# Performance work log

Measured on AMD Instinct MI355X. Metric: run time of the kernel, lower is better.

The kernel has to match this reference:

```python
import jax, jax.numpy as jnp
import numpy as np

GAMMA = 1.0        # soft-min temperature for differentiable DTW
BIG = 1e9          # value for cells outside the Sakoe-Chiba band
DTW_BW = 0.2       # band width as fraction of normalized path deviation
AVG_T_LEN = True   # divide discrepancy by input sequence length


def _softmin3(a, b, c):
    # differentiable min over the three DP predecessors
    z = jnp.stack([a, b, c], axis=0)
    return -GAMMA * jax.nn.logsumexp(-z / GAMMA, axis=0)


def _dtw(C, mask):
    """Band-limited soft-DTW DP. C: [T,K] pairwise costs, mask: [T,K] bool band.
    Returns scalar D[T-1,K-1]. Row scan over T; inner scan over K carries the
    left neighbor (recurrence D[i,j] = C[i,j] + softmin(D[i-1,j], D[i,j-1], D[i-1,j-1]))."""
    T, K = C.shape

    def row_step(carry, inp):
        prev_row, diag0 = carry            # prev_row: D[i-1,:]; diag0: virtual D[i-1,-1]
        c_row, m_row = inp
        diag = jnp.concatenate([diag0[None], prev_row[:-1]])  # D[i-1,j-1]

        def col_step(left, xs):
            c, up, dg, m = xs
            d = c + _softmin3(up, left, dg)
            d = jnp.where(m, d, BIG)       # kill cells outside the band
            return d, d

        _, row = jax.lax.scan(col_step, jnp.float32(BIG), (c_row, prev_row, diag, m_row))
        return (row, jnp.float32(BIG)), None

    # virtual border: D[-1,-1] = 0, all other border cells = BIG
    init = (jnp.full((K,), BIG, dtype=jnp.float32), jnp.float32(0.0))
    (last_row, _), _ = jax.lax.scan(row_step, init, (C, mask))
    return last_row[-1]


def setup_inputs() -> dict:
    key = jax.random.key(0)
    kx, kp = jax.random.split(key)
    B, T = 64, 512
    F, K = 32, 64
    x = jax.random.normal(kx, (B, T), dtype=jnp.float32)
    protos = jax.random.normal(kp, (F, K), dtype=jnp.float32)  # learnable DTW kernels
    return {"x": x, "protos": protos}


def reference(x, protos):
    B, T = x.shape
    F, K = protos.shape
    # pairwise squared costs: [B, F, T, K]
    C = (x[:, None, :, None] - protos[None, :, None, :]) ** 2
    # Sakoe-Chiba band on normalized coordinates
    ii = jnp.arange(T, dtype=jnp.float32) / (T - 1)
    jj = jnp.arange(K, dtype=jnp.float32) / (K - 1)
    mask = jnp.abs(ii[:, None] - jj[None, :]) <= DTW_BW  # [T, K]
    d = jax.vmap(jax.vmap(lambda c: _dtw(c, mask)))(C)    # [B, F]
    if AVG_T_LEN:
        d = d / jnp.float32(T)
    return d[:, :, None]  # [B, num_filter, out_len=1]
```

## Files before the change

kernel.cpp:

```cpp
#include <hip/hip_runtime.h>

#define T_LEN  512
#define K_LEN  64
#define NFILT  32
#define NBATCH 64
#define XOFS   64
#define XS_SZ  640
#define CHUNK  32
#define SQRT_LOG2E 1.2011224087864498f
#define LN2        0.6931471805599453f

static __device__ __forceinline__ float wave_shr1(float x) {
    int r = __builtin_amdgcn_update_dpp(0, __builtin_bit_cast(int, x),
                                        0x138, 0xF, 0xF, true);
    return __builtin_bit_cast(float, r);
}

template <int N>
static __device__ __forceinline__ float row_ror(float x) {
    int r = __builtin_amdgcn_update_dpp(0, __builtin_bit_cast(int, x),
                                        0x120 + N, 0xF, 0xF, true);
    return __builtin_bit_cast(float, r);
}

static __device__ __forceinline__ float exp2_fast(float x) {
#if __has_builtin(__builtin_amdgcn_exp2f)
    return __builtin_amdgcn_exp2f(x);
#else
    return exp2f(x);
#endif
}

__global__ __launch_bounds__(256) void dtw_kernel(const float* __restrict__ x,
                                                  const float* __restrict__ protos,
                                                  float* __restrict__ out) {
    __shared__ float xs[XS_SZ];
    const int tid  = threadIdx.x;
    const int lane = tid & 63;
    const int wid  = tid >> 6;
    const int b    = blockIdx.x >> 2;
    const int fA   = ((blockIdx.x & 3) << 2) | wid;
    const int fB   = fA + 16;

    for (int t0 = tid; t0 < XS_SZ; t0 += 256) {
        int i = t0 - XOFS;
        xs[t0] = (i >= 0 && i < T_LEN) ? x[b * T_LEN + i] * SQRT_LOG2E : 0.0f;
    }
    __syncthreads();

    const float pA = protos[fA * K_LEN + lane] * SQRT_LOG2E;
    const float pB = protos[fB * K_LEN + lane] * SQRT_LOG2E;
    const float jj = (float)lane / 63.0f;

    int a0 = 0, b0 = T_LEN - 1;
    while (a0 < b0) { int m = (a0 + b0) >> 1;
        if ((float)m / 511.0f - jj >= -0.2f) b0 = m; else a0 = m + 1; }
    const int ilo = a0;
    a0 = 0; b0 = T_LEN - 1;
    while (a0 < b0) { int m = (a0 + b0 + 1) >> 1;
        if ((float)m / 511.0f - jj <= 0.2f) a0 = m; else b0 = m - 1; }
    const int ihi = a0;

    const unsigned range = (unsigned)(ihi - ilo);
    unsigned t = (unsigned)(-(lane + ilo));
    float prevA = 0.0f, prevB = 0.0f;
    float dgpA  = (lane == 0) ? 1.0f : 0.0f;
    float dgpB  = dgpA;
    int   S2A = 0, S2B = 0;
    int   base = XOFS - lane;

    float A[CHUNK], B[CHUNK];
#pragma unroll
    for (int k = 0; k < CHUNK; ++k) A[k] = xs[base + k];

#define STEP(XV) do {                                     \
        float xv_  = (XV);                                \
        float dfA_ = xv_ - pA;                            \
        float dfB_ = xv_ - pB;                            \
        float wA_  = exp2_fast(-(dfA_ * dfA_));           \
        float wB_  = exp2_fast(-(dfB_ * dfB_));           \
        bool  in_  = (t <= range);                        \
        wA_ = in_ ? wA_ : 0.0f;                           \
        wB_ = in_ ? wB_ : 0.0f;                           \
        float aA_ = prevA + dgpA;                         \
        float aB_ = prevB + dgpB;                         \
        float lA_ = wave_shr1(prevA);                     \
        float lB_ = wave_shr1(prevB);                     \
        dgpA = lA_; dgpB = lB_;                           \
        prevA = (aA_ + lA_) * wA_;                        \
        prevB = (aB_ + lB_) * wB_;                        \
        ++t;                                              \
    } while (0)

#define RENORM_HALF(PV, DG, S2) do {                                         \
        float m_ = PV;                                                       \
        m_ = fmaxf(m_, row_ror<8>(m_));                                      \
        m_ = fmaxf(m_, row_ror<4>(m_));                                      \
        m_ = fmaxf(m_, row_ror<2>(m_));                                      \
        m_ = fmaxf(m_, row_ror<1>(m_));                                      \
        int mi_ = __builtin_bit_cast(int, m_);                               \
        unsigned r0_ = (unsigned)__builtin_amdgcn_readlane(mi_, 0);          \
        unsigned r1_ = (unsigned)__builtin_amdgcn_readlane(mi_, 16);         \
        unsigned r2_ = (unsigned)__builtin_amdgcn_readlane(mi_, 32);         \
        unsigned r3_ = (unsigned)__builtin_amdgcn_readlane(mi_, 48);         \
        unsigned ra_ = r0_ > r1_ ? r0_ : r1_;                                \
        unsigned rb_ = r2_ > r3_ ? r2_ : r3_;                                \
        unsigned mx_ = ra_ > rb_ ? ra_ : rb_;                                \
        int e_  = (int)((mx_ >> 23) & 0xFF);                                 \
        int Me_ = 284 - e_;                                                  \
        Me_ = Me_ < 1 ? 1 : (Me_ > 254 ? 254 : Me_);                         \
        float M_ = __builtin_bit_cast(float, Me_ << 23);                     \
        S2 += Me_ - 127;                                                     \
        PV *= M_;                                                            \
        DG *= M_;                                                            \
    } while (0)

#define RENORM() do { RENORM_HALF(prevA, dgpA, S2A);                         \
                      RENORM_HALF(prevB, dgpB, S2B); } while (0)

#pragma unroll 1
    for (int cc = 0; cc < 8; ++cc) {
#pragma unroll
        for (int k = 0; k < CHUNK; ++k) B[k] = xs[base + CHUNK + k];
#pragma unroll
        for (int k = 0; k < CHUNK; ++k) STEP(A[k]);
        RENORM();
        base += CHUNK;
#pragma unroll
        for (int k = 0; k < CHUNK; ++k) A[k] = xs[base + CHUNK + k];
#pragma unroll
        for (int k = 0; k < CHUNK; ++k) STEP(B[k]);
        RENORM();
        base += CHUNK;
    }
#pragma unroll
    for (int k = 0; k < CHUNK; ++k) B[k] = xs[base + CHUNK + k];
#pragma unroll
    for (int k = 0; k < CHUNK; ++k) STEP(A[k]);
    RENORM();
#pragma unroll
    for (int k = 0; k < 31; ++k) STEP(B[k]);

    if (lane == 63) {
        float DA = ((float)S2A - log2f(prevA)) * LN2;
        float DB = ((float)S2B - log2f(prevB)) * LN2;
        out[b * NFILT + fA] = DA * (1.0f / (float)T_LEN);
        out[b * NFILT + fB] = DB * (1.0f / (float)T_LEN);
    }
#undef STEP
#undef RENORM_HALF
#undef RENORM
}

extern "C" void kernel_launch(void* const* d_in, const int* in_sizes, int n_in,
                              void* d_out, int out_size, void* d_ws, size_t ws_size,
                              hipStream_t stream) {
    const float* x      = (const float*)d_in[0];
    const float* protos = (const float*)d_in[1];
    float* out          = (float*)d_out;

    dim3 grid(NBATCH * 4);
    dim3 block(256);
    hipLaunchKernelGGL(dtw_kernel, grid, block, 0, stream, x, protos, out);
}
```

Before: 29.82 us.

## Drop LDS staging; inject x via lane-0 shift register across single-wave blocks

Removes the shared-memory staging of x and the block barrier. Each block is now a single wave, and x values are loaded as uniform global reads (same address for all lanes) into registers. They enter at lane 0 and shift down the wave through DPP each step, replacing per-lane LDS reads. The band mask is folded into the exp2 argument as a large negative offset, and the x scaling is folded into an FMA. The cost is an extra DPP shift per step on the serial dependency chain, and the grid grows to 1024 one-wave blocks.

```diff
diff --git a/kernel.cpp b/kernel.cpp
--- a/kernel.cpp
+++ b/kernel.cpp
@@ -4,9 +4,6 @@
 #define K_LEN  64
 #define NFILT  32
 #define NBATCH 64
-#define XOFS   64
-#define XS_SZ  640
-#define CHUNK  32
 #define SQRT_LOG2E 1.2011224087864498f
 #define LN2        0.6931471805599453f
 
@@ -31,26 +28,20 @@
 #endif
 }
 
-__global__ __launch_bounds__(256) void dtw_kernel(const float* __restrict__ x,
-                                                  const float* __restrict__ protos,
-                                                  float* __restrict__ out) {
-    __shared__ float xs[XS_SZ];
-    const int tid  = threadIdx.x;
-    const int lane = tid & 63;
-    const int wid  = tid >> 6;
-    const int b    = blockIdx.x >> 2;
-    const int fA   = ((blockIdx.x & 3) << 2) | wid;
+__global__ __launch_bounds__(64) void dtw_kernel(const float* __restrict__ x,
+                                                 const float* __restrict__ protos,
+                                                 float* __restrict__ out) {
+    const int lane = threadIdx.x & 63;
+    const int b    = blockIdx.x >> 4;
+    const int fA   = blockIdx.x & 15;
     const int fB   = fA + 16;
 
-    for (int t0 = tid; t0 < XS_SZ; t0 += 256) {
-        int i = t0 - XOFS;
-        xs[t0] = (i >= 0 && i < T_LEN) ? x[b * T_LEN + i] * SQRT_LOG2E : 0.0f;
-    }
-    __syncthreads();
+    const float* __restrict__ xr = x + b * T_LEN;
 
-    const float pA = protos[fA * K_LEN + lane] * SQRT_LOG2E;
-    const float pB = protos[fB * K_LEN + lane] * SQRT_LOG2E;
-    const float jj = (float)lane / 63.0f;
+    const float pAn = -protos[fA * K_LEN + lane] * SQRT_LOG2E;
+    const float pBn = -protos[fB * K_LEN + lane] * SQRT_LOG2E;
+    const float jj  = (float)lane / 63.0f;
+    const bool lane0 = (lane == 0);
 
     int a0 = 0, b0 = T_LEN - 1;
     while (a0 < b0) { int m = (a0 + b0) >> 1;
@@ -63,33 +54,37 @@
 
     const unsigned range = (unsigned)(ihi - ilo);
     unsigned t = (unsigned)(-(lane + ilo));
+    float xv    = 0.0f;
     float prevA = 0.0f, prevB = 0.0f;
-    float dgpA  = (lane == 0) ? 1.0f : 0.0f;
+    float dgpA  = lane0 ? 1.0f : 0.0f;
     float dgpB  = dgpA;
     int   S2A = 0, S2B = 0;
-    int   base = XOFS - lane;
 
-    float A[CHUNK], B[CHUNK];
-#pragma unroll
-    for (int k = 0; k < CHUNK; ++k) A[k] = xs[base + k];
+#define STEP_BODY() do {                                        \
+        float sel_ = (t <= range) ? 0.0f : -3.0e38f;            \
+        ++t;                                                    \
+        float dsA_ = __builtin_fmaf(xv, SQRT_LOG2E, pAn);       \
+        float dsB_ = __builtin_fmaf(xv, SQRT_LOG2E, pBn);       \
+        float wA_  = exp2_fast(__builtin_fmaf(dsA_, -dsA_, sel_)); \
+        float wB_  = exp2_fast(__builtin_fmaf(dsB_, -dsB_, sel_)); \
+        float lA_  = wave_shr1(prevA);                          \
+        float lB_  = wave_shr1(prevB);                          \
+        float aA_  = prevA + dgpA;                              \
+        float aB_  = prevB + dgpB;                              \
+        dgpA = lA_; dgpB = lB_;                                 \
+        prevA = (aA_ + lA_) * wA_;                              \
+        prevB = (aB_ + lB_) * wB_;                              \
+    } while (0)
 
-#define STEP(XV) do {                                     \
-        float xv_  = (XV);                                \
-        float dfA_ = xv_ - pA;                            \
-        float dfB_ = xv_ - pB;                            \
-        float wA_  = exp2_fast(-(dfA_ * dfA_));           \
-        float wB_  = exp2_fast(-(dfB_ * dfB_));           \
-        bool  in_  = (t <= range);                        \
-        wA_ = in_ ? wA_ : 0.0f;                           \
-        wB_ = in_ ? wB_ : 0.0f;                           \
-        float aA_ = prevA + dgpA;                         \
-        float aB_ = prevB + dgpB;                         \
-        float lA_ = wave_shr1(prevA);                     \
-        float lB_ = wave_shr1(prevB);                     \
-        dgpA = lA_; dgpB = lB_;                           \
-        prevA = (aA_ + lA_) * wA_;                        \
-        prevB = (aB_ + lB_) * wB_;                        \
-        ++t;                                              \
+#define STEP_INJ(SK) do {                                       \
+        float xs_ = wave_shr1(xv);                              \
+        xv = lane0 ? (SK) : xs_;                                \
+        STEP_BODY();                                            \
+    } while (0)
+
+#define STEP_TAIL() do {                                        \
+        xv = wave_shr1(xv);    \
+        STEP_BODY();                                            \
     } while (0)
 
 #define RENORM_HALF(PV, DG, S2) do {                                         \
@@ -118,28 +113,30 @@
 #define RENORM() do { RENORM_HALF(prevA, dgpA, S2A);                         \
                       RENORM_HALF(prevB, dgpB, S2B); } while (0)
 
+    float SA[32], SB[32];
+#pragma unroll
+    for (int k = 0; k < 32; ++k) SA[k] = xr[k];
+
 #pragma unroll 1
-    for (int cc = 0; cc < 8; ++cc) {
+    for (int c = 0; c < 8; ++c) {
+        const int o1 = (2 * c + 1) * 32;
 #pragma unroll
-        for (int k = 0; k < CHUNK; ++k) B[k] = xs[base + CHUNK + k];
+        for (int k = 0; k < 32; ++k) SB[k] = xr[o1 + k];
 #pragma unroll
-        for (int k = 0; k < CHUNK; ++k) STEP(A[k]);
+        for (int k = 0; k < 32; ++k) STEP_INJ(SA[k]);
         RENORM();
-        base += CHUNK;
+        const int o2 = (2 * c + 2 < 16) ? (2 * c + 2) * 32 : 15 * 32;
 #pragma unroll
-        for (int k = 0; k < CHUNK; ++k) A[k] = xs[base + CHUNK + k];
+        for (int k = 0; k < 32; ++k) SA[k] = xr[o2 + k];
 #pragma unroll
-        for (int k = 0; k < CHUNK; ++k) STEP(B[k]);
+        for (int k = 0; k < 32; ++k) STEP_INJ(SB[k]);
         RENORM();
-        base += CHUNK;
     }
 #pragma unroll
-    for (int k = 0; k < CHUNK; ++k) B[k] = xs[base + CHUNK + k];
-#pragma unroll
-    for (int k = 0; k < CHUNK; ++k) STEP(A[k]);
+    for (int k = 0; k < 32; ++k) STEP_TAIL();
     RENORM();
 #pragma unroll
-    for (int k = 0; k < 31; ++k) STEP(B[k]);
+    for (int k = 0; k < 31; ++k) STEP_TAIL();
 
     if (lane == 63) {
         float DA = ((float)S2A - log2f(prevA)) * LN2;
@@ -147,7 +144,9 @@
         out[b * NFILT + fA] = DA * (1.0f / (float)T_LEN);
         out[b * NFILT + fB] = DB * (1.0f / (float)T_LEN);
     }
-#undef STEP
+#undef STEP_BODY
+#undef STEP_INJ
+#undef STEP_TAIL
 #undef RENORM_HALF
 #undef RENORM
 }
@@ -159,7 +158,7 @@
     const float* protos = (const float*)d_in[1];
     float* out          = (float*)d_out;
 
-    dim3 grid(NBATCH * 4);
-    dim3 block(256);
+    dim3 grid(NBATCH * 16);
+    dim3 block(64);
     hipLaunchKernelGGL(dtw_kernel, grid, block, 0, stream, x, protos, out);
 }
```

Result: no change. 29.85 us (+0.1%).
